# Kernel tuning notes

Measured on AMD Instinct MI355X. Metric: run time of the kernel, lower is better.

Reference implementation:

```python
import jax, jax.numpy as jnp
import numpy as np

EPS = 1e-5

def layer_norm(x, gamma, beta):
    mu = jnp.mean(x, axis=-1, keepdims=True)
    var = jnp.mean(jnp.square(x - mu), axis=-1, keepdims=True)
    return (x - mu) * jax.lax.rsqrt(var + EPS) * gamma + beta

def reverse_sigmoid(x):
    # torch version clamps value to [0.001, 0.999] with a detached offset ->
    # straight-through: clipped value, identity gradient into the logit.
    y = x + jax.lax.stop_gradient(jnp.clip(x, 0.001, 0.999) - x)
    return jnp.log(y) - jnp.log1p(-y)

def setup_inputs() -> dict:
    key = jax.random.key(0)
    ks = jax.random.split(key, 8)
    N, D, A, F8, FD = 32768, 1024, 256, 8, 64
    inp = {
        "unary_term": jax.random.normal(ks[0], (N, D), jnp.float32),
        "pair_term": jax.random.normal(ks[1], (N, D), jnp.float32),
        "auxiliary_term": jax.random.normal(ks[2], (N, A), jnp.float32),
        "auxiliary_gating_weight": jax.random.uniform(ks[3], (N,), jnp.float32),
        # self.w params: LayerNorm(2D) + Linear(2D, FD)
        "ln_gamma": jnp.ones((2 * D,), jnp.float32),
        "ln_beta": jnp.zeros((2 * D,), jnp.float32),
        "W": jax.random.normal(ks[4], (2 * D, FD), jnp.float32) * 0.02,
        "b": jnp.zeros((FD,), jnp.float32),
        # self.w_aux params: LayerNorm(A) + Linear(A, 8)
        "ln_aux_gamma": jnp.ones((A,), jnp.float32),
        "ln_aux_beta": jnp.zeros((A,), jnp.float32),
        "W_aux": jax.random.normal(ks[5], (A, F8), jnp.float32) * 0.02,
        "b_aux": jnp.zeros((F8,), jnp.float32),
        # use_auxiliary_gate_weight=True -> both init to 0.33
        "gate_weight": jnp.array(0.33, jnp.float32),
        "aux_gate_weight": jnp.array(0.33, jnp.float32),
    }
    return inp

def reference(unary_term, pair_term, auxiliary_term, auxiliary_gating_weight,
              ln_gamma, ln_beta, W, b, ln_aux_gamma, ln_aux_beta, W_aux, b_aux,
              gate_weight, aux_gate_weight):
    # paired_feats = relu(cat([unary, pair], 1))
    paired = jax.nn.relu(jnp.concatenate([unary_term, pair_term], axis=1))  # [N, 2D]
    # gate = sigmoid(Linear(relu(LN(paired))))
    gate = jax.nn.sigmoid(jax.nn.relu(layer_norm(paired, ln_gamma, ln_beta)) @ W + b)  # [N, FD]
    aux_gate = jax.nn.sigmoid(jax.nn.relu(layer_norm(auxiliary_term, ln_aux_gamma, ln_aux_beta)) @ W_aux + b_aux)  # [N, 8]
    gate = jnp.mean(gate, axis=1)        # [N]
    aux_gate = jnp.mean(aux_gate, axis=1)  # [N]
    logit = gate_weight * reverse_sigmoid(gate) + aux_gate_weight * reverse_sigmoid(aux_gate)
    g = jax.nn.sigmoid(logit) * auxiliary_gating_weight  # use_auxiliary_gate_weight=True
    output = pair_term * g[:, None]
    return (output, g)
```

## Files before the change

kernel.cpp:

```cpp
#include <hip/hip_runtime.h>
#include <math.h>


#define EPS_LN 1e-5f

typedef __attribute__((ext_vector_type(8))) short short8;
typedef __attribute__((ext_vector_type(4))) float f32x4;

__device__ __forceinline__ unsigned short f2bf(float f) {
  unsigned int u = __float_as_uint(f);
  u += 0x7FFFu + ((u >> 16) & 1u);
  return (unsigned short)(u >> 16);
}

__device__ __forceinline__ unsigned pkbf2(float a, float b) {
  unsigned ua = __float_as_uint(a), ub = __float_as_uint(b);
  ua += 0x7FFFu + ((ua >> 16) & 1u);
  ub += 0x7FFFu + ((ub >> 16) & 1u);
  return (ub & 0xFFFF0000u) | (ua >> 16);
}

union S8U { unsigned u[4]; short8 v; };

__device__ __forceinline__ short8 pack8(float x0, float x1, float x2, float x3,
                                        float x4, float x5, float x6, float x7) {
  S8U r;
  r.u[0] = pkbf2(x0, x1); r.u[1] = pkbf2(x2, x3);
  r.u[2] = pkbf2(x4, x5); r.u[3] = pkbf2(x6, x7);
  return r.v;
}

__device__ __forceinline__ short8 ones8() {
  S8U r; r.u[0] = r.u[1] = r.u[2] = r.u[3] = 0x3F803F80u;
  return r.v;
}

__device__ __forceinline__ float sigmoidf_(float x) {
  return 1.0f / (1.0f + __expf(-x));
}

__device__ __forceinline__ float rsigf(float x) {
  float y = fminf(fmaxf(x, 0.001f), 0.999f);
  return logf(y) - log1pf(-y);
}

__global__ void prep_frags(const float* __restrict__ W,
                           const float* __restrict__ W_aux,
                           unsigned short* __restrict__ wfrag) {
  const int lane = threadIdx.x;
  const int b = blockIdx.x;
  unsigned short tmp[8];
  if (b < 256) {
    const int ntile = b >> 6;
    const int kb = b & 63;
    const int f = (ntile << 4) + (lane & 15);
    const int kbase = (kb << 5) + ((lane >> 4) << 3);
#pragma unroll
    for (int j = 0; j < 8; ++j) tmp[j] = f2bf(W[(size_t)(kbase + j) * 64 + f]);
    ushort4* dst = reinterpret_cast<ushort4*>(wfrag + (((size_t)b * 64 + lane) << 3));
    dst[0] = make_ushort4(tmp[0], tmp[1], tmp[2], tmp[3]);
    dst[1] = make_ushort4(tmp[4], tmp[5], tmp[6], tmp[7]);
  } else {
    const int kb = b - 256;
    const int f = lane & 15;
    const int kbase = (kb << 5) + ((lane >> 4) << 3);
#pragma unroll
    for (int j = 0; j < 8; ++j)
      tmp[j] = (f < 8) ? f2bf(W_aux[(size_t)(kbase + j) * 8 + f]) : (unsigned short)0;
    ushort4* dst = reinterpret_cast<ushort4*>(wfrag + 131072 +
                                              (((size_t)kb * 64 + lane) << 3));
    dst[0] = make_ushort4(tmp[0], tmp[1], tmp[2], tmp[3]);
    dst[1] = make_ushort4(tmp[4], tmp[5], tmp[6], tmp[7]);
  }
}

__global__ void __launch_bounds__(256, 4) fused_main(
    const float* __restrict__ unary, const float* __restrict__ pair,
    const float* __restrict__ aux, const float* __restrict__ auxw,
    const float* __restrict__ ln_g, const float* __restrict__ ln_b,
    const float* __restrict__ b_lin,
    const float* __restrict__ ln_ag, const float* __restrict__ ln_ab,
    const float* __restrict__ b_aux,
    const float* __restrict__ gw, const float* __restrict__ agw,
    const unsigned short* __restrict__ wfrag,
    float* __restrict__ out, float* __restrict__ out_g) {
  __shared__ float part[4][16][68];
  __shared__ float auxpart[4][16][8];
  __shared__ float4 statp[4][16];

  const int tid = threadIdx.x;
  const int w = tid >> 6;
  const int lane = tid & 63;
  const int base = blockIdx.x << 4;
  const int m = lane & 15;
  const int q = lane >> 4;

  const float* srcp = (w < 2) ? unary : pair;
  const float* arow = srcp + (size_t)(base + m) * 1024 + ((w & 1) << 9) + (q << 3);
  const float* axrow = aux + (size_t)(base + m) * 256 + (w << 6) + (q << 3);

  const short8 onef = ones8();

  f32x4 aS = {0.f,0.f,0.f,0.f}, aQ = {0.f,0.f,0.f,0.f};
  f32x4 sS = {0.f,0.f,0.f,0.f}, sQ = {0.f,0.f,0.f,0.f};
  float axv[16];
  short8 ar[16];

#pragma unroll
  for (int kb = 0; kb < 2; ++kb) {
    const float4 x0 = *reinterpret_cast<const float4*>(axrow + (kb << 5));
    const float4 x1 = *reinterpret_cast<const float4*>(axrow + (kb << 5) + 4);
    axv[kb * 8 + 0] = x0.x; axv[kb * 8 + 1] = x0.y;
    axv[kb * 8 + 2] = x0.z; axv[kb * 8 + 3] = x0.w;
    axv[kb * 8 + 4] = x1.x; axv[kb * 8 + 5] = x1.y;
    axv[kb * 8 + 6] = x1.z; axv[kb * 8 + 7] = x1.w;
    const short8 a = pack8(x0.x, x0.y, x0.z, x0.w, x1.x, x1.y, x1.z, x1.w);
    const short8 a2 = pack8(x0.x * x0.x, x0.y * x0.y, x0.z * x0.z, x0.w * x0.w,
                            x1.x * x1.x, x1.y * x1.y, x1.z * x1.z, x1.w * x1.w);
    sS = __builtin_amdgcn_mfma_f32_16x16x32_bf16(a, onef, sS, 0, 0, 0);
    sQ = __builtin_amdgcn_mfma_f32_16x16x32_bf16(a2, onef, sQ, 0, 0, 0);
  }

#pragma unroll
  for (int kb = 0; kb < 16; ++kb) {
    const float4 x0 = *reinterpret_cast<const float4*>(arow + (kb << 5));
    const float4 x1 = *reinterpret_cast<const float4*>(arow + (kb << 5) + 4);
    const float r0 = fmaxf(x0.x, 0.f), r1 = fmaxf(x0.y, 0.f);
    const float r2 = fmaxf(x0.z, 0.f), r3 = fmaxf(x0.w, 0.f);
    const float r4 = fmaxf(x1.x, 0.f), r5 = fmaxf(x1.y, 0.f);
    const float r6 = fmaxf(x1.z, 0.f), r7 = fmaxf(x1.w, 0.f);
    ar[kb] = pack8(r0, r1, r2, r3, r4, r5, r6, r7);
    const short8 a2 = pack8(r0 * r0, r1 * r1, r2 * r2, r3 * r3,
                            r4 * r4, r5 * r5, r6 * r6, r7 * r7);
    aS = __builtin_amdgcn_mfma_f32_16x16x32_bf16(ar[kb], onef, aS, 0, 0, 0);
    aQ = __builtin_amdgcn_mfma_f32_16x16x32_bf16(a2, onef, aQ, 0, 0, 0);
  }

  if ((lane & 15) == 0) {
    statp[w][(q << 2) + 0] = make_float4(aS[0], aQ[0], sS[0], sQ[0]);
    statp[w][(q << 2) + 1] = make_float4(aS[1], aQ[1], sS[1], sQ[1]);
    statp[w][(q << 2) + 2] = make_float4(aS[2], aQ[2], sS[2], sQ[2]);
    statp[w][(q << 2) + 3] = make_float4(aS[3], aQ[3], sS[3], sQ[3]);
  }
  __syncthreads();

  const float4 s0 = statp[0][m], s1 = statp[1][m], s2 = statp[2][m], s3 = statp[3][m];
  const float S  = s0.x + s1.x + s2.x + s3.x;
  const float Q  = s0.y + s1.y + s2.y + s3.y;
  const float Sa = s0.z + s1.z + s2.z + s3.z;
  const float Qa = s0.w + s1.w + s2.w + s3.w;
  const float mu = S * (1.f / 2048.f);
  const float rs = rsqrtf(Q * (1.f / 2048.f) - mu * mu + EPS_LN);
  const float nmr = -mu * rs;
  const float amu = Sa * (1.f / 256.f);
  const float ars = rsqrtf(Qa * (1.f / 256.f) - amu * amu + EPS_LN);
  const float anmr = -amu * ars;

  const float* gp = ln_g + (w << 9) + (q << 3);
  const float* bp = ln_b + (w << 9) + (q << 3);
  const unsigned short* wfp = wfrag + ((size_t)((w << 4) * 64 + lane) << 3);

  f32x4 acc[4] = {{0.f,0.f,0.f,0.f},{0.f,0.f,0.f,0.f},
                  {0.f,0.f,0.f,0.f},{0.f,0.f,0.f,0.f}};
#pragma unroll
  for (int kb = 0; kb < 16; ++kb) {
    const float4 g0 = *reinterpret_cast<const float4*>(gp + (kb << 5));
    const float4 g1 = *reinterpret_cast<const float4*>(gp + (kb << 5) + 4);
    const float4 b0 = *reinterpret_cast<const float4*>(bp + (kb << 5));
    const float4 b1 = *reinterpret_cast<const float4*>(bp + (kb << 5) + 4);
    S8U u; u.v = ar[kb];
    const float r0 = __uint_as_float(u.u[0] << 16);
    const float r1 = __uint_as_float(u.u[0] & 0xFFFF0000u);
    const float r2 = __uint_as_float(u.u[1] << 16);
    const float r3 = __uint_as_float(u.u[1] & 0xFFFF0000u);
    const float r4 = __uint_as_float(u.u[2] << 16);
    const float r5 = __uint_as_float(u.u[2] & 0xFFFF0000u);
    const float r6 = __uint_as_float(u.u[3] << 16);
    const float r7 = __uint_as_float(u.u[3] & 0xFFFF0000u);
    const float n0 = fmaf(r0, rs, nmr), n1 = fmaf(r1, rs, nmr);
    const float n2 = fmaf(r2, rs, nmr), n3 = fmaf(r3, rs, nmr);
    const float n4 = fmaf(r4, rs, nmr), n5 = fmaf(r5, rs, nmr);
    const float n6 = fmaf(r6, rs, nmr), n7 = fmaf(r7, rs, nmr);
    const short8 af = pack8(
        fmaxf(fmaf(n0, g0.x, b0.x), 0.f), fmaxf(fmaf(n1, g0.y, b0.y), 0.f),
        fmaxf(fmaf(n2, g0.z, b0.z), 0.f), fmaxf(fmaf(n3, g0.w, b0.w), 0.f),
        fmaxf(fmaf(n4, g1.x, b1.x), 0.f), fmaxf(fmaf(n5, g1.y, b1.y), 0.f),
        fmaxf(fmaf(n6, g1.z, b1.z), 0.f), fmaxf(fmaf(n7, g1.w, b1.w), 0.f));
#pragma unroll
    for (int nt = 0; nt < 4; ++nt) {
      const short8 bf = *reinterpret_cast<const short8*>(
          wfp + (size_t)nt * 32768 + (kb << 9));
      acc[nt] = __builtin_amdgcn_mfma_f32_16x16x32_bf16(af, bf, acc[nt], 0, 0, 0);
    }
  }

  const float* agp = ln_ag + (w << 6) + (q << 3);
  const float* abp = ln_ab + (w << 6) + (q << 3);
  const unsigned short* afp = wfrag + 131072;
  f32x4 acca = {0.f,0.f,0.f,0.f};
#pragma unroll
  for (int kb = 0; kb < 2; ++kb) {
    const float4 g0 = *reinterpret_cast<const float4*>(agp + (kb << 5));
    const float4 g1 = *reinterpret_cast<const float4*>(agp + (kb << 5) + 4);
    const float4 b0 = *reinterpret_cast<const float4*>(abp + (kb << 5));
    const float4 b1 = *reinterpret_cast<const float4*>(abp + (kb << 5) + 4);
    short8 af;
    af[0] = (short)f2bf(fmaxf(fmaf(fmaf(axv[kb*8+0], ars, anmr), g0.x, b0.x), 0.f));
    af[1] = (short)f2bf(fmaxf(fmaf(fmaf(axv[kb*8+1], ars, anmr), g0.y, b0.y), 0.f));
    af[2] = (short)f2bf(fmaxf(fmaf(fmaf(axv[kb*8+2], ars, anmr), g0.z, b0.z), 0.f));
    af[3] = (short)f2bf(fmaxf(fmaf(fmaf(axv[kb*8+3], ars, anmr), g0.w, b0.w), 0.f));
    af[4] = (short)f2bf(fmaxf(fmaf(fmaf(axv[kb*8+4], ars, anmr), g1.x, b1.x), 0.f));
    af[5] = (short)f2bf(fmaxf(fmaf(fmaf(axv[kb*8+5], ars, anmr), g1.y, b1.y), 0.f));
    af[6] = (short)f2bf(fmaxf(fmaf(fmaf(axv[kb*8+6], ars, anmr), g1.z, b1.z), 0.f));
    af[7] = (short)f2bf(fmaxf(fmaf(fmaf(axv[kb*8+7], ars, anmr), g1.w, b1.w), 0.f));
    const short8 bf = *reinterpret_cast<const short8*>(
        afp + ((size_t)(((w << 1) + kb) * 64 + lane) << 3));
    acca = __builtin_amdgcn_mfma_f32_16x16x32_bf16(af, bf, acca, 0, 0, 0);
  }

#pragma unroll
  for (int nt = 0; nt < 4; ++nt)
#pragma unroll
    for (int r = 0; r < 4; ++r)
      part[w][(q << 2) + r][(nt << 4) + m] = acc[nt][r];
  if (m < 8) {
#pragma unroll
    for (int r = 0; r < 4; ++r)
      auxpart[w][(q << 2) + r][m] = acca[r];
  }
  __syncthreads();

  const int rl = (w << 2) + q;
  const int f0 = m << 2;
  const float4 p0 = *reinterpret_cast<const float4*>(&part[0][rl][f0]);
  const float4 p1 = *reinterpret_cast<const float4*>(&part[1][rl][f0]);
  const float4 p2 = *reinterpret_cast<const float4*>(&part[2][rl][f0]);
  const float4 p3 = *reinterpret_cast<const float4*>(&part[3][rl][f0]);
  const float4 blv = reinterpret_cast<const float4*>(b_lin)[m];
  float sgs = sigmoidf_(p0.x + p1.x + p2.x + p3.x + blv.x)
            + sigmoidf_(p0.y + p1.y + p2.y + p3.y + blv.y)
            + sigmoidf_(p0.z + p1.z + p2.z + p3.z + blv.z)
            + sigmoidf_(p0.w + p1.w + p2.w + p3.w + blv.w);
  sgs += __shfl_xor(sgs, 1);
  sgs += __shfl_xor(sgs, 2);
  sgs += __shfl_xor(sgs, 4);
  sgs += __shfl_xor(sgs, 8);
  const float gate = sgs * (1.f / 64.f);

  const int fa = m & 7;
  float av4 = auxpart[0][rl][fa] + auxpart[1][rl][fa] +
              auxpart[2][rl][fa] + auxpart[3][rl][fa];
  float axs = sigmoidf_(av4 + b_aux[fa]);
  axs = (m < 8) ? axs : 0.f;
  axs += __shfl_xor(axs, 1);
  axs += __shfl_xor(axs, 2);
  axs += __shfl_xor(axs, 4);
  axs += __shfl_xor(axs, 8);
  const float auxg = axs * 0.125f;

  const float logit = gw[0] * rsigf(gate) + agw[0] * rsigf(auxg);
  const float g = sigmoidf_(logit) * auxw[base + rl];
  if (m == 0) out_g[base + rl] = g;

#pragma unroll
  for (int i = 0; i < 4; ++i) {
    const float gi = __shfl(g, (i << 4));
    const int row = base + (w << 2) + i;
    const float4* pp = reinterpret_cast<const float4*>(pair + (size_t)row * 1024);
    float4* oo = reinterpret_cast<float4*>(out + (size_t)row * 1024);
#pragma unroll
    for (int j = 0; j < 4; ++j) {
      float4 pv = pp[lane + (j << 6)];
      pv.x *= gi; pv.y *= gi; pv.z *= gi; pv.w *= gi;
      oo[lane + (j << 6)] = pv;
    }
  }
}

extern "C" void kernel_launch(void* const* d_in, const int* in_sizes, int n_in,
                              void* d_out, int out_size, void* d_ws, size_t ws_size,
                              hipStream_t stream) {
  const float* unary = (const float*)d_in[0];
  const float* pair  = (const float*)d_in[1];
  const float* aux   = (const float*)d_in[2];
  const float* auxw  = (const float*)d_in[3];
  const float* ln_g  = (const float*)d_in[4];
  const float* ln_b  = (const float*)d_in[5];
  const float* W     = (const float*)d_in[6];
  const float* b     = (const float*)d_in[7];
  const float* ln_ag = (const float*)d_in[8];
  const float* ln_ab = (const float*)d_in[9];
  const float* W_aux = (const float*)d_in[10];
  const float* b_aux = (const float*)d_in[11];
  const float* gw    = (const float*)d_in[12];
  const float* agw   = (const float*)d_in[13];

  const int N = in_sizes[3];
  unsigned short* wfrag = (unsigned short*)d_ws;
  float* out = (float*)d_out;
  float* out_g = out + (size_t)N * 1024;

  prep_frags<<<264, 64, 0, stream>>>(W, W_aux, wfrag);
  fused_main<<<N / 16, 256, 0, stream>>>(unary, pair, aux, auxw, ln_g, ln_b, b,
                                         ln_ag, ln_ab, b_aux, gw, agw,
                                         wfrag, out, out_g);
}
```

Before: 449.0 us.

## Give each wave full-K rows, dropping LDS reductions and block barriers

Each wave now owns 8 rows and loops over the whole 2048-wide K dimension itself, instead of four waves splitting K across 16 rows. This removes the shared-memory partial sums, both __syncthreads, and the 16-entry register cache of bf16 activations. Statistics are broadcast across lanes with shuffles, and the gate reductions are done in registers. In exchange, unary and pair rows are read from memory twice (once for the LN statistics, once for the GEMM). Because only 8 distinct rows fill each 16-row MFMA tile, half of the matrix-core work is redundant.

```diff
diff --git a/kernel.cpp b/kernel.cpp
--- a/kernel.cpp
+++ b/kernel.cpp
@@ -42,6 +42,13 @@
 __device__ __forceinline__ float rsigf(float x) {
   float y = fminf(fmaxf(x, 0.001f), 0.999f);
   return logf(y) - log1pf(-y);
+}
+
+__device__ __forceinline__ float bcast_row(const f32x4 v, int m) {
+  const float v01 = (m & 1) ? v[1] : v[0];
+  const float v23 = (m & 1) ? v[3] : v[2];
+  const float vs  = (m & 2) ? v23 : v01;
+  return __shfl(vs, ((m & 4) << 2) + (m & 3));
 }
 
 __global__ void prep_frags(const float* __restrict__ W,
@@ -84,36 +91,27 @@
     const float* __restrict__ gw, const float* __restrict__ agw,
     const unsigned short* __restrict__ wfrag,
     float* __restrict__ out, float* __restrict__ out_g) {
-  __shared__ float part[4][16][68];
-  __shared__ float auxpart[4][16][8];
-  __shared__ float4 statp[4][16];
-
   const int tid = threadIdx.x;
   const int w = tid >> 6;
   const int lane = tid & 63;
-  const int base = blockIdx.x << 4;
   const int m = lane & 15;
   const int q = lane >> 4;
-
-  const float* srcp = (w < 2) ? unary : pair;
-  const float* arow = srcp + (size_t)(base + m) * 1024 + ((w & 1) << 9) + (q << 3);
-  const float* axrow = aux + (size_t)(base + m) * 256 + (w << 6) + (q << 3);
-
+  const int rb = ((blockIdx.x << 2) + w) << 3;
+  const int r8 = m & 7;
+
+  const size_t xo = ((size_t)(rb + r8) << 10) + (q << 3);
+  const float* urow = unary + xo;
+  const float* prow = pair + xo;
+  const float* axrow = aux + ((size_t)(rb + r8) << 8) + (q << 3);
   const short8 onef = ones8();
 
+  f32x4 sS = {0.f,0.f,0.f,0.f}, sQ = {0.f,0.f,0.f,0.f};
   f32x4 aS = {0.f,0.f,0.f,0.f}, aQ = {0.f,0.f,0.f,0.f};
-  f32x4 sS = {0.f,0.f,0.f,0.f}, sQ = {0.f,0.f,0.f,0.f};
-  float axv[16];
-  short8 ar[16];
-
-#pragma unroll
-  for (int kb = 0; kb < 2; ++kb) {
+
+#pragma unroll
+  for (int kb = 0; kb < 8; ++kb) {
     const float4 x0 = *reinterpret_cast<const float4*>(axrow + (kb << 5));
     const float4 x1 = *reinterpret_cast<const float4*>(axrow + (kb << 5) + 4);
-    axv[kb * 8 + 0] = x0.x; axv[kb * 8 + 1] = x0.y;
-    axv[kb * 8 + 2] = x0.z; axv[kb * 8 + 3] = x0.w;
-    axv[kb * 8 + 4] = x1.x; axv[kb * 8 + 5] = x1.y;
-    axv[kb * 8 + 6] = x1.z; axv[kb * 8 + 7] = x1.w;
     const short8 a = pack8(x0.x, x0.y, x0.z, x0.w, x1.x, x1.y, x1.z, x1.w);
     const short8 a2 = pack8(x0.x * x0.x, x0.y * x0.y, x0.z * x0.z, x0.w * x0.w,
                             x1.x * x1.x, x1.y * x1.y, x1.z * x1.z, x1.w * x1.w);
@@ -121,34 +119,39 @@
     sQ = __builtin_amdgcn_mfma_f32_16x16x32_bf16(a2, onef, sQ, 0, 0, 0);
   }
 
-#pragma unroll
-  for (int kb = 0; kb < 16; ++kb) {
-    const float4 x0 = *reinterpret_cast<const float4*>(arow + (kb << 5));
-    const float4 x1 = *reinterpret_cast<const float4*>(arow + (kb << 5) + 4);
+#pragma unroll 4
+  for (int kb = 0; kb < 32; ++kb) {
+    const float4 x0 = *reinterpret_cast<const float4*>(urow + (kb << 5));
+    const float4 x1 = *reinterpret_cast<const float4*>(urow + (kb << 5) + 4);
     const float r0 = fmaxf(x0.x, 0.f), r1 = fmaxf(x0.y, 0.f);
     const float r2 = fmaxf(x0.z, 0.f), r3 = fmaxf(x0.w, 0.f);
     const float r4 = fmaxf(x1.x, 0.f), r5 = fmaxf(x1.y, 0.f);
     const float r6 = fmaxf(x1.z, 0.f), r7 = fmaxf(x1.w, 0.f);
-    ar[kb] = pack8(r0, r1, r2, r3, r4, r5, r6, r7);
+    const short8 a = pack8(r0, r1, r2, r3, r4, r5, r6, r7);
     const short8 a2 = pack8(r0 * r0, r1 * r1, r2 * r2, r3 * r3,
                             r4 * r4, r5 * r5, r6 * r6, r7 * r7);
-    aS = __builtin_amdgcn_mfma_f32_16x16x32_bf16(ar[kb], onef, aS, 0, 0, 0);
+    aS = __builtin_amdgcn_mfma_f32_16x16x32_bf16(a, onef, aS, 0, 0, 0);
     aQ = __builtin_amdgcn_mfma_f32_16x16x32_bf16(a2, onef, aQ, 0, 0, 0);
   }
-
-  if ((lane & 15) == 0) {
-    statp[w][(q << 2) + 0] = make_float4(aS[0], aQ[0], sS[0], sQ[0]);
-    statp[w][(q << 2) + 1] = make_float4(aS[1], aQ[1], sS[1], sQ[1]);
-    statp[w][(q << 2) + 2] = make_float4(aS[2], aQ[2], sS[2], sQ[2]);
-    statp[w][(q << 2) + 3] = make_float4(aS[3], aQ[3], sS[3], sQ[3]);
-  }
-  __syncthreads();
-
-  const float4 s0 = statp[0][m], s1 = statp[1][m], s2 = statp[2][m], s3 = statp[3][m];
-  const float S  = s0.x + s1.x + s2.x + s3.x;
-  const float Q  = s0.y + s1.y + s2.y + s3.y;
-  const float Sa = s0.z + s1.z + s2.z + s3.z;
-  const float Qa = s0.w + s1.w + s2.w + s3.w;
+#pragma unroll 4
+  for (int kb = 0; kb < 32; ++kb) {
+    const float4 x0 = *reinterpret_cast<const float4*>(prow + (kb << 5));
+    const float4 x1 = *reinterpret_cast<const float4*>(prow + (kb << 5) + 4);
+    const float r0 = fmaxf(x0.x, 0.f), r1 = fmaxf(x0.y, 0.f);
+    const float r2 = fmaxf(x0.z, 0.f), r3 = fmaxf(x0.w, 0.f);
+    const float r4 = fmaxf(x1.x, 0.f), r5 = fmaxf(x1.y, 0.f);
+    const float r6 = fmaxf(x1.z, 0.f), r7 = fmaxf(x1.w, 0.f);
+    const short8 a = pack8(r0, r1, r2, r3, r4, r5, r6, r7);
+    const short8 a2 = pack8(r0 * r0, r1 * r1, r2 * r2, r3 * r3,
+                            r4 * r4, r5 * r5, r6 * r6, r7 * r7);
+    aS = __builtin_amdgcn_mfma_f32_16x16x32_bf16(a, onef, aS, 0, 0, 0);
+    aQ = __builtin_amdgcn_mfma_f32_16x16x32_bf16(a2, onef, aQ, 0, 0, 0);
+  }
+
+  const float S  = bcast_row(aS, m);
+  const float Q  = bcast_row(aQ, m);
+  const float Sa = bcast_row(sS, m);
+  const float Qa = bcast_row(sQ, m);
   const float mu = S * (1.f / 2048.f);
   const float rs = rsqrtf(Q * (1.f / 2048.f) - mu * mu + EPS_LN);
   const float nmr = -mu * rs;
@@ -156,31 +159,28 @@
   const float ars = rsqrtf(Qa * (1.f / 256.f) - amu * amu + EPS_LN);
   const float anmr = -amu * ars;
 
-  const float* gp = ln_g + (w << 9) + (q << 3);
-  const float* bp = ln_b + (w << 9) + (q << 3);
-  const unsigned short* wfp = wfrag + ((size_t)((w << 4) * 64 + lane) << 3);
-
   f32x4 acc[4] = {{0.f,0.f,0.f,0.f},{0.f,0.f,0.f,0.f},
                   {0.f,0.f,0.f,0.f},{0.f,0.f,0.f,0.f}};
-#pragma unroll
-  for (int kb = 0; kb < 16; ++kb) {
-    const float4 g0 = *reinterpret_cast<const float4*>(gp + (kb << 5));
-    const float4 g1 = *reinterpret_cast<const float4*>(gp + (kb << 5) + 4);
-    const float4 b0 = *reinterpret_cast<const float4*>(bp + (kb << 5));
-    const float4 b1 = *reinterpret_cast<const float4*>(bp + (kb << 5) + 4);
-    S8U u; u.v = ar[kb];
-    const float r0 = __uint_as_float(u.u[0] << 16);
-    const float r1 = __uint_as_float(u.u[0] & 0xFFFF0000u);
-    const float r2 = __uint_as_float(u.u[1] << 16);
-    const float r3 = __uint_as_float(u.u[1] & 0xFFFF0000u);
-    const float r4 = __uint_as_float(u.u[2] << 16);
-    const float r5 = __uint_as_float(u.u[2] & 0xFFFF0000u);
-    const float r6 = __uint_as_float(u.u[3] << 16);
-    const float r7 = __uint_as_float(u.u[3] & 0xFFFF0000u);
-    const float n0 = fmaf(r0, rs, nmr), n1 = fmaf(r1, rs, nmr);
-    const float n2 = fmaf(r2, rs, nmr), n3 = fmaf(r3, rs, nmr);
-    const float n4 = fmaf(r4, rs, nmr), n5 = fmaf(r5, rs, nmr);
-    const float n6 = fmaf(r6, rs, nmr), n7 = fmaf(r7, rs, nmr);
+  const int qo = q << 3;
+
+#pragma unroll 2
+  for (int kb = 0; kb < 32; ++kb) {
+    const float4 x0 = *reinterpret_cast<const float4*>(urow + (kb << 5));
+    const float4 x1 = *reinterpret_cast<const float4*>(urow + (kb << 5) + 4);
+    const float* gp = ln_g + (kb << 5) + qo;
+    const float* bp = ln_b + (kb << 5) + qo;
+    const float4 g0 = *reinterpret_cast<const float4*>(gp);
+    const float4 g1 = *reinterpret_cast<const float4*>(gp + 4);
+    const float4 b0 = *reinterpret_cast<const float4*>(bp);
+    const float4 b1 = *reinterpret_cast<const float4*>(bp + 4);
+    const float n0 = fmaf(fmaxf(x0.x, 0.f), rs, nmr);
+    const float n1 = fmaf(fmaxf(x0.y, 0.f), rs, nmr);
+    const float n2 = fmaf(fmaxf(x0.z, 0.f), rs, nmr);
+    const float n3 = fmaf(fmaxf(x0.w, 0.f), rs, nmr);
+    const float n4 = fmaf(fmaxf(x1.x, 0.f), rs, nmr);
+    const float n5 = fmaf(fmaxf(x1.y, 0.f), rs, nmr);
+    const float n6 = fmaf(fmaxf(x1.z, 0.f), rs, nmr);
+    const float n7 = fmaf(fmaxf(x1.w, 0.f), rs, nmr);
     const short8 af = pack8(
         fmaxf(fmaf(n0, g0.x, b0.x), 0.f), fmaxf(fmaf(n1, g0.y, b0.y), 0.f),
         fmaxf(fmaf(n2, g0.z, b0.z), 0.f), fmaxf(fmaf(n3, g0.w, b0.w), 0.f),
@@ -189,85 +189,125 @@
 #pragma unroll
     for (int nt = 0; nt < 4; ++nt) {
       const short8 bf = *reinterpret_cast<const short8*>(
-          wfp + (size_t)nt * 32768 + (kb << 9));
+          wfrag + (((size_t)(nt << 6) + kb) << 9) + (lane << 3));
       acc[nt] = __builtin_amdgcn_mfma_f32_16x16x32_bf16(af, bf, acc[nt], 0, 0, 0);
     }
   }
-
-  const float* agp = ln_ag + (w << 6) + (q << 3);
-  const float* abp = ln_ab + (w << 6) + (q << 3);
-  const unsigned short* afp = wfrag + 131072;
+#pragma unroll 2
+  for (int kb = 0; kb < 32; ++kb) {
+    const float4 x0 = *reinterpret_cast<const float4*>(prow + (kb << 5));
+    const float4 x1 = *reinterpret_cast<const float4*>(prow + (kb << 5) + 4);
+    const float* gp = ln_g + 1024 + (kb << 5) + qo;
+    const float* bp = ln_b + 1024 + (kb << 5) + qo;
+    const float4 g0 = *reinterpret_cast<const float4*>(gp);
+    const float4 g1 = *reinterpret_cast<const float4*>(gp + 4);
+    const float4 b0 = *reinterpret_cast<const float4*>(bp);
+    const float4 b1 = *reinterpret_cast<const float4*>(bp + 4);
+    const float n0 = fmaf(fmaxf(x0.x, 0.f), rs, nmr);
+    const float n1 = fmaf(fmaxf(x0.y, 0.f), rs, nmr);
+    const float n2 = fmaf(fmaxf(x0.z, 0.f), rs, nmr);
+    const float n3 = fmaf(fmaxf(x0.w, 0.f), rs, nmr);
+    const float n4 = fmaf(fmaxf(x1.x, 0.f), rs, nmr);
+    const float n5 = fmaf(fmaxf(x1.y, 0.f), rs, nmr);
+    const float n6 = fmaf(fmaxf(x1.z, 0.f), rs, nmr);
+    const float n7 = fmaf(fmaxf(x1.w, 0.f), rs, nmr);
+    const short8 af = pack8(
+        fmaxf(fmaf(n0, g0.x, b0.x), 0.f), fmaxf(fmaf(n1, g0.y, b0.y), 0.f),
+        fmaxf(fmaf(n2, g0.z, b0.z), 0.f), fmaxf(fmaf(n3, g0.w, b0.w), 0.f),
+        fmaxf(fmaf(n4, g1.x, b1.x), 0.f), fmaxf(fmaf(n5, g1.y, b1.y), 0.f),
+        fmaxf(fmaf(n6, g1.z, b1.z), 0.f), fmaxf(fmaf(n7, g1.w, b1.w), 0.f));
+#pragma unroll
+    for (int nt = 0; nt < 4; ++nt) {
+      const short8 bf = *reinterpret_cast<const short8*>(
+          wfrag + (((size_t)(nt << 6) + (kb + 32)) << 9) + (lane << 3));
+      acc[nt] = __builtin_amdgcn_mfma_f32_16x16x32_bf16(af, bf, acc[nt], 0, 0, 0);
+    }
+  }
+
   f32x4 acca = {0.f,0.f,0.f,0.f};
 #pragma unroll
-  for (int kb = 0; kb < 2; ++kb) {
-    const float4 g0 = *reinterpret_cast<const float4*>(agp + (kb << 5));
-    const float4 g1 = *reinterpret_cast<const float4*>(agp + (kb << 5) + 4);
-    const float4 b0 = *reinterpret_cast<const float4*>(abp + (kb << 5));
-    const float4 b1 = *reinterpret_cast<const float4*>(abp + (kb << 5) + 4);
-    short8 af;
-    af[0] = (short)f2bf(fmaxf(fmaf(fmaf(axv[kb*8+0], ars, anmr), g0.x, b0.x), 0.f));
-    af[1] = (short)f2bf(fmaxf(fmaf(fmaf(axv[kb*8+1], ars, anmr), g0.y, b0.y), 0.f));
-    af[2] = (short)f2bf(fmaxf(fmaf(fmaf(axv[kb*8+2], ars, anmr), g0.z, b0.z), 0.f));
-    af[3] = (short)f2bf(fmaxf(fmaf(fmaf(axv[kb*8+3], ars, anmr), g0.w, b0.w), 0.f));
-    af[4] = (short)f2bf(fmaxf(fmaf(fmaf(axv[kb*8+4], ars, anmr), g1.x, b1.x), 0.f));
-    af[5] = (short)f2bf(fmaxf(fmaf(fmaf(axv[kb*8+5], ars, anmr), g1.y, b1.y), 0.f));
-    af[6] = (short)f2bf(fmaxf(fmaf(fmaf(axv[kb*8+6], ars, anmr), g1.z, b1.z), 0.f));
-    af[7] = (short)f2bf(fmaxf(fmaf(fmaf(axv[kb*8+7], ars, anmr), g1.w, b1.w), 0.f));
+  for (int kb = 0; kb < 8; ++kb) {
+    const float4 x0 = *reinterpret_cast<const float4*>(axrow + (kb << 5));
+    const float4 x1 = *reinterpret_cast<const float4*>(axrow + (kb << 5) + 4);
+    const float* gp = ln_ag + (kb << 5) + qo;
+    const float* bp = ln_ab + (kb << 5) + qo;
+    const float4 g0 = *reinterpret_cast<const float4*>(gp);
+    const float4 g1 = *reinterpret_cast<const float4*>(gp + 4);
+    const float4 b0 = *reinterpret_cast<const float4*>(bp);
+    const float4 b1 = *reinterpret_cast<const float4*>(bp + 4);
+    const short8 af = pack8(
+        fmaxf(fmaf(fmaf(x0.x, ars, anmr), g0.x, b0.x), 0.f),
+        fmaxf(fmaf(fmaf(x0.y, ars, anmr), g0.y, b0.y), 0.f),
+        fmaxf(fmaf(fmaf(x0.z, ars, anmr), g0.z, b0.z), 0.f),
+        fmaxf(fmaf(fmaf(x0.w, ars, anmr), g0.w, b0.w), 0.f),
+        fmaxf(fmaf(fmaf(x1.x, ars, anmr), g1.x, b1.x), 0.f),
+        fmaxf(fmaf(fmaf(x1.y, ars, anmr), g1.y, b1.y), 0.f),
+        fmaxf(fmaf(fmaf(x1.z, ars, anmr), g1.z, b1.z), 0.f),
+        fmaxf(fmaf(fmaf(x1.w, ars, anmr), g1.w, b1.w), 0.f));
     const short8 bf = *reinterpret_cast<const short8*>(
-        afp + ((size_t)(((w << 1) + kb) * 64 + lane) << 3));
+        wfrag + 131072 + (((size_t)(kb << 6) + lane) << 3));
     acca = __builtin_amdgcn_mfma_f32_16x16x32_bf16(af, bf, acca, 0, 0, 0);
   }
 
-#pragma unroll
-  for (int nt = 0; nt < 4; ++nt)
-#pragma unroll
-    for (int r = 0; r < 4; ++r)
-      part[w][(q << 2) + r][(nt << 4) + m] = acc[nt][r];
-  if (m < 8) {
-#pragma unroll
-    for (int r = 0; r < 4; ++r)
-      auxpart[w][(q << 2) + r][m] = acca[r];
-  }
-  __syncthreads();
-
-  const int rl = (w << 2) + q;
-  const int f0 = m << 2;
-  const float4 p0 = *reinterpret_cast<const float4*>(&part[0][rl][f0]);
-  const float4 p1 = *reinterpret_cast<const float4*>(&part[1][rl][f0]);
-  const float4 p2 = *reinterpret_cast<const float4*>(&part[2][rl][f0]);
-  const float4 p3 = *reinterpret_cast<const float4*>(&part[3][rl][f0]);
-  const float4 blv = reinterpret_cast<const float4*>(b_lin)[m];
-  float sgs = sigmoidf_(p0.x + p1.x + p2.x + p3.x + blv.x)
-            + sigmoidf_(p0.y + p1.y + p2.y + p3.y + blv.y)
-            + sigmoidf_(p0.z + p1.z + p2.z + p3.z + blv.z)
-            + sigmoidf_(p0.w + p1.w + p2.w + p3.w + blv.w);
-  sgs += __shfl_xor(sgs, 1);
-  sgs += __shfl_xor(sgs, 2);
-  sgs += __shfl_xor(sgs, 4);
-  sgs += __shfl_xor(sgs, 8);
-  const float gate = sgs * (1.f / 64.f);
-
-  const int fa = m & 7;
-  float av4 = auxpart[0][rl][fa] + auxpart[1][rl][fa] +
-              auxpart[2][rl][fa] + auxpart[3][rl][fa];
-  float axs = sigmoidf_(av4 + b_aux[fa]);
-  axs = (m < 8) ? axs : 0.f;
-  axs += __shfl_xor(axs, 1);
-  axs += __shfl_xor(axs, 2);
-  axs += __shfl_xor(axs, 4);
-  axs += __shfl_xor(axs, 8);
-  const float auxg = axs * 0.125f;
-
-  const float logit = gw[0] * rsigf(gate) + agw[0] * rsigf(auxg);
-  const float g = sigmoidf_(logit) * auxw[base + rl];
-  if (m == 0) out_g[base + rl] = g;
-
+  const float bl0 = b_lin[m], bl1 = b_lin[16 + m];
+  const float bl2 = b_lin[32 + m], bl3 = b_lin[48 + m];
+  const float ba = b_aux[m & 7];
+  float srow[4], arow[4];
+#pragma unroll
+  for (int r = 0; r < 4; ++r) {
+    float t = sigmoidf_(acc[0][r] + bl0) + sigmoidf_(acc[1][r] + bl1) +
+              sigmoidf_(acc[2][r] + bl2) + sigmoidf_(acc[3][r] + bl3);
+    t += __shfl_xor(t, 1);
+    t += __shfl_xor(t, 2);
+    t += __shfl_xor(t, 4);
+    t += __shfl_xor(t, 8);
+    srow[r] = t;
+    float u = (m < 8) ? sigmoidf_(acca[r] + ba) : 0.f;
+    u += __shfl_xor(u, 1);
+    u += __shfl_xor(u, 2);
+    u += __shfl_xor(u, 4);
+    u += __shfl_xor(u, 8);
+    arow[r] = u;
+  }
+  const bool qodd = (q & 1) != 0;
+  float glo[4], ghi[4], alo[4], ahi[4];
+#pragma unroll
+  for (int r = 0; r < 4; ++r) {
+    const float so = __shfl(srow[r], lane ^ 16);
+    const float ao = __shfl(arow[r], lane ^ 16);
+    glo[r] = qodd ? so : srow[r];
+    ghi[r] = qodd ? srow[r] : so;
+    alo[r] = qodd ? ao : arow[r];
+    ahi[r] = qodd ? arow[r] : ao;
+  }
+
+  const float gwt = gw[0];
+  const float agwt = agw[0];
+  float gq[8];
 #pragma unroll
   for (int i = 0; i < 4; ++i) {
-    const float gi = __shfl(g, (i << 4));
-    const int row = base + (w << 2) + i;
-    const float4* pp = reinterpret_cast<const float4*>(pair + (size_t)row * 1024);
-    float4* oo = reinterpret_cast<float4*>(out + (size_t)row * 1024);
+    const float gate = glo[i] * (1.f / 64.f);
+    const float auxg = alo[i] * (1.f / 8.f);
+    const float logit = gwt * rsigf(gate) + agwt * rsigf(auxg);
+    gq[i] = sigmoidf_(logit) * auxw[rb + i];
+  }
+#pragma unroll
+  for (int i = 0; i < 4; ++i) {
+    const float gate = ghi[i] * (1.f / 64.f);
+    const float auxg = ahi[i] * (1.f / 8.f);
+    const float logit = gwt * rsigf(gate) + agwt * rsigf(auxg);
+    gq[4 + i] = sigmoidf_(logit) * auxw[rb + 4 + i];
+  }
+  if (lane == 0) {
+#pragma unroll
+    for (int i = 0; i < 8; ++i) out_g[rb + i] = gq[i];
+  }
+
+#pragma unroll
+  for (int i = 0; i < 8; ++i) {
+    const float gi = gq[i];
+    const float4* pp = reinterpret_cast<const float4*>(pair + ((size_t)(rb + i) << 10));
+    float4* oo = reinterpret_cast<float4*>(out + ((size_t)(rb + i) << 10));
 #pragma unroll
     for (int j = 0; j < 4; ++j) {
       float4 pv = pp[lane + (j << 6)];
@@ -301,7 +341,7 @@
   float* out_g = out + (size_t)N * 1024;
 
   prep_frags<<<264, 64, 0, stream>>>(W, W_aux, wfrag);
-  fused_main<<<N / 16, 256, 0, stream>>>(unary, pair, aux, auxw, ln_g, ln_b, b,
+  fused_main<<<N / 32, 256, 0, stream>>>(unary, pair, aux, auxw, ln_g, ln_b, b,
                                          ln_ag, ln_ab, b_aux, gw, agw,
                                          wfrag, out, out_g);
 }
```

Measured after the change: 526.1 us. 17.2% more time.

## Drop cached bf16 activations, reload from global in reverse order, raise occupancy

Applied to the files above, without the earlier changes.

Stops holding the 16 packed bf16 activation fragments in registers between the statistics pass and the GEMM pass. The GEMM loop now re-reads the fp32 inputs from global memory, walking the k-blocks in reverse so the most recently read data is still in cache, which frees registers so launch bounds can go from 4 to 5 waves per SIMD. It also gets sum-of-squares from an MFMA of a with itself instead of packing squares, uses the hardware packed bf16 conversion intrinsic, and simplifies the stats store. The cost is extra global/L2 traffic and slightly different rounding, since squares are now formed from bf16 values.

```diff
diff --git a/kernel.cpp b/kernel.cpp
--- a/kernel.cpp
+++ b/kernel.cpp
@@ -1,4 +1,5 @@
 #include <hip/hip_runtime.h>
+#include <hip/hip_bf16.h>
 #include <math.h>
 
 
@@ -14,10 +15,9 @@
 }
 
 __device__ __forceinline__ unsigned pkbf2(float a, float b) {
-  unsigned ua = __float_as_uint(a), ub = __float_as_uint(b);
-  ua += 0x7FFFu + ((ua >> 16) & 1u);
-  ub += 0x7FFFu + ((ub >> 16) & 1u);
-  return (ub & 0xFFFF0000u) | (ua >> 16);
+  union { __hip_bfloat162 h; unsigned u; } c;
+  c.h = __float22bfloat162_rn(make_float2(a, b));
+  return c.u;
 }
 
 union S8U { unsigned u[4]; short8 v; };
@@ -74,7 +74,7 @@
   }
 }
 
-__global__ void __launch_bounds__(256, 4) fused_main(
+__global__ void __launch_bounds__(256, 5) fused_main(
     const float* __restrict__ unary, const float* __restrict__ pair,
     const float* __restrict__ aux, const float* __restrict__ auxw,
     const float* __restrict__ ln_g, const float* __restrict__ ln_b,
@@ -104,7 +104,6 @@
   f32x4 aS = {0.f,0.f,0.f,0.f}, aQ = {0.f,0.f,0.f,0.f};
   f32x4 sS = {0.f,0.f,0.f,0.f}, sQ = {0.f,0.f,0.f,0.f};
   float axv[16];
-  short8 ar[16];
 
 #pragma unroll
   for (int kb = 0; kb < 2; ++kb) {
@@ -115,32 +114,26 @@
     axv[kb * 8 + 4] = x1.x; axv[kb * 8 + 5] = x1.y;
     axv[kb * 8 + 6] = x1.z; axv[kb * 8 + 7] = x1.w;
     const short8 a = pack8(x0.x, x0.y, x0.z, x0.w, x1.x, x1.y, x1.z, x1.w);
-    const short8 a2 = pack8(x0.x * x0.x, x0.y * x0.y, x0.z * x0.z, x0.w * x0.w,
-                            x1.x * x1.x, x1.y * x1.y, x1.z * x1.z, x1.w * x1.w);
     sS = __builtin_amdgcn_mfma_f32_16x16x32_bf16(a, onef, sS, 0, 0, 0);
-    sQ = __builtin_amdgcn_mfma_f32_16x16x32_bf16(a2, onef, sQ, 0, 0, 0);
+    sQ = __builtin_amdgcn_mfma_f32_16x16x32_bf16(a, a, sQ, 0, 0, 0);
   }
 
 #pragma unroll
   for (int kb = 0; kb < 16; ++kb) {
     const float4 x0 = *reinterpret_cast<const float4*>(arow + (kb << 5));
     const float4 x1 = *reinterpret_cast<const float4*>(arow + (kb << 5) + 4);
-    const float r0 = fmaxf(x0.x, 0.f), r1 = fmaxf(x0.y, 0.f);
-    const float r2 = fmaxf(x0.z, 0.f), r3 = fmaxf(x0.w, 0.f);
-    const float r4 = fmaxf(x1.x, 0.f), r5 = fmaxf(x1.y, 0.f);
-    const float r6 = fmaxf(x1.z, 0.f), r7 = fmaxf(x1.w, 0.f);
-    ar[kb] = pack8(r0, r1, r2, r3, r4, r5, r6, r7);
-    const short8 a2 = pack8(r0 * r0, r1 * r1, r2 * r2, r3 * r3,
-                            r4 * r4, r5 * r5, r6 * r6, r7 * r7);
-    aS = __builtin_amdgcn_mfma_f32_16x16x32_bf16(ar[kb], onef, aS, 0, 0, 0);
-    aQ = __builtin_amdgcn_mfma_f32_16x16x32_bf16(a2, onef, aQ, 0, 0, 0);
-  }
-
-  if ((lane & 15) == 0) {
-    statp[w][(q << 2) + 0] = make_float4(aS[0], aQ[0], sS[0], sQ[0]);
-    statp[w][(q << 2) + 1] = make_float4(aS[1], aQ[1], sS[1], sQ[1]);
-    statp[w][(q << 2) + 2] = make_float4(aS[2], aQ[2], sS[2], sQ[2]);
-    statp[w][(q << 2) + 3] = make_float4(aS[3], aQ[3], sS[3], sQ[3]);
+    const short8 a = pack8(fmaxf(x0.x, 0.f), fmaxf(x0.y, 0.f),
+                           fmaxf(x0.z, 0.f), fmaxf(x0.w, 0.f),
+                           fmaxf(x1.x, 0.f), fmaxf(x1.y, 0.f),
+                           fmaxf(x1.z, 0.f), fmaxf(x1.w, 0.f));
+    aS = __builtin_amdgcn_mfma_f32_16x16x32_bf16(a, onef, aS, 0, 0, 0);
+    aQ = __builtin_amdgcn_mfma_f32_16x16x32_bf16(a, a, aQ, 0, 0, 0);
+  }
+
+  const int col = lane & 15;
+  if ((col >> 2) == q) {
+    const int r = col & 3;
+    statp[w][col] = make_float4(aS[r], aQ[r], sS[r], sQ[r]);
   }
   __syncthreads();
 
@@ -163,24 +156,22 @@
   f32x4 acc[4] = {{0.f,0.f,0.f,0.f},{0.f,0.f,0.f,0.f},
                   {0.f,0.f,0.f,0.f},{0.f,0.f,0.f,0.f}};
 #pragma unroll
-  for (int kb = 0; kb < 16; ++kb) {
+  for (int kr = 0; kr < 16; ++kr) {
+    const int kb = 15 - kr;
+    const float4 x0 = *reinterpret_cast<const float4*>(arow + (kb << 5));
+    const float4 x1 = *reinterpret_cast<const float4*>(arow + (kb << 5) + 4);
     const float4 g0 = *reinterpret_cast<const float4*>(gp + (kb << 5));
     const float4 g1 = *reinterpret_cast<const float4*>(gp + (kb << 5) + 4);
     const float4 b0 = *reinterpret_cast<const float4*>(bp + (kb << 5));
     const float4 b1 = *reinterpret_cast<const float4*>(bp + (kb << 5) + 4);
-    S8U u; u.v = ar[kb];
-    const float r0 = __uint_as_float(u.u[0] << 16);
-    const float r1 = __uint_as_float(u.u[0] & 0xFFFF0000u);
-    const float r2 = __uint_as_float(u.u[1] << 16);
-    const float r3 = __uint_as_float(u.u[1] & 0xFFFF0000u);
-    const float r4 = __uint_as_float(u.u[2] << 16);
-    const float r5 = __uint_as_float(u.u[2] & 0xFFFF0000u);
-    const float r6 = __uint_as_float(u.u[3] << 16);
-    const float r7 = __uint_as_float(u.u[3] & 0xFFFF0000u);
-    const float n0 = fmaf(r0, rs, nmr), n1 = fmaf(r1, rs, nmr);
-    const float n2 = fmaf(r2, rs, nmr), n3 = fmaf(r3, rs, nmr);
-    const float n4 = fmaf(r4, rs, nmr), n5 = fmaf(r5, rs, nmr);
-    const float n6 = fmaf(r6, rs, nmr), n7 = fmaf(r7, rs, nmr);
+    const float n0 = fmaf(fmaxf(x0.x, 0.f), rs, nmr);
+    const float n1 = fmaf(fmaxf(x0.y, 0.f), rs, nmr);
+    const float n2 = fmaf(fmaxf(x0.z, 0.f), rs, nmr);
+    const float n3 = fmaf(fmaxf(x0.w, 0.f), rs, nmr);
+    const float n4 = fmaf(fmaxf(x1.x, 0.f), rs, nmr);
+    const float n5 = fmaf(fmaxf(x1.y, 0.f), rs, nmr);
+    const float n6 = fmaf(fmaxf(x1.z, 0.f), rs, nmr);
+    const float n7 = fmaf(fmaxf(x1.w, 0.f), rs, nmr);
     const short8 af = pack8(
         fmaxf(fmaf(n0, g0.x, b0.x), 0.f), fmaxf(fmaf(n1, g0.y, b0.y), 0.f),
         fmaxf(fmaf(n2, g0.z, b0.z), 0.f), fmaxf(fmaf(n3, g0.w, b0.w), 0.f),
@@ -204,15 +195,15 @@
     const float4 g1 = *reinterpret_cast<const float4*>(agp + (kb << 5) + 4);
     const float4 b0 = *reinterpret_cast<const float4*>(abp + (kb << 5));
     const float4 b1 = *reinterpret_cast<const float4*>(abp + (kb << 5) + 4);
-    short8 af;
-    af[0] = (short)f2bf(fmaxf(fmaf(fmaf(axv[kb*8+0], ars, anmr), g0.x, b0.x), 0.f));
-    af[1] = (short)f2bf(fmaxf(fmaf(fmaf(axv[kb*8+1], ars, anmr), g0.y, b0.y), 0.f));
-    af[2] = (short)f2bf(fmaxf(fmaf(fmaf(axv[kb*8+2], ars, anmr), g0.z, b0.z), 0.f));
-    af[3] = (short)f2bf(fmaxf(fmaf(fmaf(axv[kb*8+3], ars, anmr), g0.w, b0.w), 0.f));
-    af[4] = (short)f2bf(fmaxf(fmaf(fmaf(axv[kb*8+4], ars, anmr), g1.x, b1.x), 0.f));
-    af[5] = (short)f2bf(fmaxf(fmaf(fmaf(axv[kb*8+5], ars, anmr), g1.y, b1.y), 0.f));
-    af[6] = (short)f2bf(fmaxf(fmaf(fmaf(axv[kb*8+6], ars, anmr), g1.z, b1.z), 0.f));
-    af[7] = (short)f2bf(fmaxf(fmaf(fmaf(axv[kb*8+7], ars, anmr), g1.w, b1.w), 0.f));
+    const short8 af = pack8(
+        fmaxf(fmaf(fmaf(axv[kb*8+0], ars, anmr), g0.x, b0.x), 0.f),
+        fmaxf(fmaf(fmaf(axv[kb*8+1], ars, anmr), g0.y, b0.y), 0.f),
+        fmaxf(fmaf(fmaf(axv[kb*8+2], ars, anmr), g0.z, b0.z), 0.f),
+        fmaxf(fmaf(fmaf(axv[kb*8+3], ars, anmr), g0.w, b0.w), 0.f),
+        fmaxf(fmaf(fmaf(axv[kb*8+4], ars, anmr), g1.x, b1.x), 0.f),
+        fmaxf(fmaf(fmaf(axv[kb*8+5], ars, anmr), g1.y, b1.y), 0.f),
+        fmaxf(fmaf(fmaf(axv[kb*8+6], ars, anmr), g1.z, b1.z), 0.f),
+        fmaxf(fmaf(fmaf(axv[kb*8+7], ars, anmr), g1.w, b1.w), 0.f));
     const short8 bf = *reinterpret_cast<const short8*>(
         afp + ((size_t)(((w << 1) + kb) * 64 + lane) << 3));
     acca = __builtin_amdgcn_mfma_f32_16x16x32_bf16(af, bf, acca, 0, 0, 0);
```

Measured after the change: 439.1 us. -2.2%, faster.
